# Performance work log

Hardware: AMD Instinct MI355X
Metric: run time of the kernel (lower is better)

Reference implementation:

```python
import jax, jax.numpy as jnp
import numpy as np

EPS = 1e-8

def setup_inputs() -> dict:
    key = jax.random.key(0)
    k1, k2 = jax.random.split(key)
    x = jax.random.normal(k1, (8192, 256), dtype=jnp.float32)
    y = jax.random.normal(k2, (8192, 256), dtype=jnp.float32)
    return {"x": x, "y": y}

def _compute_loss(a, b):
    # a: [N, d], b: [N, d]; sim = a @ b.T -> [N, N]
    sim = jnp.einsum('nd,md->nm', a, b)
    # log(exp(diag)/sum_j exp(sim_j)) = diag - logsumexp(row)  (same math as
    # exp -> diag/sum -> log in the original, expressed in fused stable form)
    pos = jnp.diagonal(sim)
    log_ratio = pos - jax.nn.logsumexp(sim, axis=1)
    return -jnp.sum(log_ratio)

def reference(x, y):
    x_norm = x / (jnp.linalg.norm(x, axis=1, keepdims=True) + EPS)
    y_norm = y / (jnp.linalg.norm(y, axis=1, keepdims=True) + EPS)
    loss_1 = _compute_loss(x_norm, x_norm)
    loss_2 = _compute_loss(x_norm, y_norm)
    loss_3 = _compute_loss(y_norm, y_norm)
    return loss_1 + loss_2 + loss_3
```

## Files before the change

### kernel.cpp

```cpp
#include <hip/hip_runtime.h>
#include <hip/hip_bf16.h>


#define N_ROWS 8192
#define DIM 256
#define EPSF 1e-8f
#define BM 128
#define BK 32
#define TILE (BM * BK)

typedef __attribute__((ext_vector_type(8))) short bf16x8;
typedef __attribute__((ext_vector_type(4))) float f32x4;
typedef __attribute__((ext_vector_type(4))) short short4v;

__device__ __forceinline__ short f2bf(float f) {
  unsigned u = __float_as_uint(f);
  unsigned r = (u + 0x7fffu + ((u >> 16) & 1u)) >> 16;
  return (short)r;
}

__device__ __forceinline__ float bf2f(short s) {
  return __uint_as_float(((unsigned)(unsigned short)s) << 16);
}

typedef const __attribute__((address_space(1))) void g_void;
typedef __attribute__((address_space(3))) void s_void;

__device__ __forceinline__ void gld_lds16(const void* g, void* l) {
  __builtin_amdgcn_global_load_lds((g_void*)g, (s_void*)l, 16, 0, 0);
}

__global__ void k_normalize(const float* __restrict__ x, const float* __restrict__ y,
                            short* __restrict__ xn, short* __restrict__ yn,
                            float* __restrict__ rowsum, float* __restrict__ out) {
  if (blockIdx.x < 96) rowsum[blockIdx.x * 256 + threadIdx.x] = 0.f;
  if (blockIdx.x == 96 && threadIdx.x == 0) out[0] = 0.f;

  int wave = threadIdx.x >> 6;
  int lane = threadIdx.x & 63;
  int row = blockIdx.x * 4 + wave;
  const float* src;
  short* dst;
  int r;
  if (row < N_ROWS) { src = x; dst = xn; r = row; }
  else              { src = y; dst = yn; r = row - N_ROWS; }
  const float4 v = *(const float4*)(src + r * DIM + lane * 4);
  float ss = v.x * v.x + v.y * v.y + v.z * v.z + v.w * v.w;
  #pragma unroll
  for (int m = 1; m < 64; m <<= 1) ss += __shfl_xor(ss, m, 64);
  float scale = 1.0f / (sqrtf(ss) + EPSF);
  short4v o;
  o.x = f2bf(v.x * scale);
  o.y = f2bf(v.y * scale);
  o.z = f2bf(v.z * scale);
  o.w = f2bf(v.w * scale);
  *(short4v*)(dst + r * DIM + lane * 4) = o;
}

__global__ __launch_bounds__(256, 4) void k_gemm(const short* __restrict__ xn,
                                                 const short* __restrict__ yn,
                                                 float* __restrict__ rowsum) {
  __shared__ __align__(16) short As[2 * TILE];
  __shared__ __align__(16) short Bs[2 * TILE];
  __shared__ float redbuf[256];

  int bid = blockIdx.x;
  int swz = (bid & 7) * 1032 + (bid >> 3);

  int pair, mb, nb;
  if (swz < 4160) {
    pair = (swz < 2080) ? 0 : 2;
    int t = (swz < 2080) ? swz : swz - 2080;
    int r = 0;
    while (t >= 64 - r) { t -= 64 - r; ++r; }
    mb = r; nb = r + t;
  } else {
    pair = 1;
    int t = swz - 4160;
    mb = t >> 6; nb = t & 63;
  }

  const short* Ap = (pair == 2) ? yn : xn;
  const short* Bp = (pair == 0) ? xn : yn;
  const short* Abase = Ap + mb * BM * DIM;
  const short* Bbase = Bp + nb * BM * DIM;

  int tid = threadIdx.x;
  int lane = tid & 63;
  int wid = tid >> 6;
  int wm = wid >> 1, wn = wid & 1;

  redbuf[tid] = 0.f;

  f32x4 acc[4][4];
  #pragma unroll
  for (int i = 0; i < 4; ++i)
    #pragma unroll
    for (int j = 0; j < 4; ++j) acc[i][j] = (f32x4){0.f, 0.f, 0.f, 0.f};

  auto stage = [&](int buf, int koff) {
    #pragma unroll
    for (int i = 0; i < 2; ++i) {
      int s = i * 256 + tid;
      int row = s >> 2, c = s & 3;
      int cs = c ^ (row & 3) ^ ((row >> 2) & 3);
      gld_lds16(Abase + row * DIM + koff + cs * 8, As + buf * TILE + s * 8);
      gld_lds16(Bbase + row * DIM + koff + cs * 8, Bs + buf * TILE + s * 8);
    }
  };

  int fslot = (lane >> 4) ^ (lane & 3) ^ ((lane >> 2) & 3);

  auto compute = [&](int buf) {
    bf16x8 a[4], b[4];
    #pragma unroll
    for (int mi = 0; mi < 4; ++mi) {
      int row = wm * 64 + mi * 16 + (lane & 15);
      a[mi] = *(const bf16x8*)(As + buf * TILE + row * BK + fslot * 8);
    }
    #pragma unroll
    for (int ni = 0; ni < 4; ++ni) {
      int row = wn * 64 + ni * 16 + (lane & 15);
      b[ni] = *(const bf16x8*)(Bs + buf * TILE + row * BK + fslot * 8);
    }
    #pragma unroll
    for (int mi = 0; mi < 4; ++mi)
      #pragma unroll
      for (int ni = 0; ni < 4; ++ni)
        acc[mi][ni] = __builtin_amdgcn_mfma_f32_16x16x32_bf16(a[mi], b[ni], acc[mi][ni], 0, 0, 0);
  };

  stage(0, 0);
  __syncthreads();
  #pragma unroll
  for (int ks = 0; ks < 8; ++ks) {
    if (ks < 7) stage((ks + 1) & 1, (ks + 1) * BK);
    compute(ks & 1);
    if (ks < 7) __syncthreads();
  }

  #pragma unroll
  for (int mi = 0; mi < 4; ++mi)
    #pragma unroll
    for (int ni = 0; ni < 4; ++ni)
      #pragma unroll
      for (int r = 0; r < 4; ++r)
        acc[mi][ni][r] = __expf(acc[mi][ni][r]);

  float rs[4][4];
  #pragma unroll
  for (int mi = 0; mi < 4; ++mi)
    #pragma unroll
    for (int r = 0; r < 4; ++r)
      rs[mi][r] = acc[mi][0][r] + acc[mi][1][r] + acc[mi][2][r] + acc[mi][3][r];
  #pragma unroll
  for (int m = 1; m < 16; m <<= 1)
    #pragma unroll
    for (int mi = 0; mi < 4; ++mi)
      #pragma unroll
      for (int r = 0; r < 4; ++r) rs[mi][r] += __shfl_xor(rs[mi][r], m, 64);
  if ((lane & 15) == 0) {
    int rloc = wm * 64 + (lane >> 4) * 4;
    #pragma unroll
    for (int mi = 0; mi < 4; ++mi)
      #pragma unroll
      for (int r = 0; r < 4; ++r)
        atomicAdd(&redbuf[rloc + mi * 16 + r], rs[mi][r]);
  }

  bool do_cols = (pair != 1) && (nb > mb);
  if (do_cols) {
    float cs[4];
    #pragma unroll
    for (int ni = 0; ni < 4; ++ni) {
      cs[ni] = 0.f;
      #pragma unroll
      for (int mi = 0; mi < 4; ++mi)
        #pragma unroll
        for (int r = 0; r < 4; ++r) cs[ni] += acc[mi][ni][r];
    }
    #pragma unroll
    for (int m = 16; m < 64; m <<= 1)
      #pragma unroll
      for (int ni = 0; ni < 4; ++ni) cs[ni] += __shfl_xor(cs[ni], m, 64);
    if (lane < 16) {
      #pragma unroll
      for (int ni = 0; ni < 4; ++ni)
        atomicAdd(&redbuf[128 + wn * 64 + ni * 16 + lane], cs[ni]);
    }
  }
  __syncthreads();

  if (tid < 128)
    atomicAdd(&rowsum[pair * N_ROWS + mb * BM + tid], redbuf[tid]);
  else if (do_cols)
    atomicAdd(&rowsum[pair * N_ROWS + nb * BM + (tid - 128)], redbuf[tid]);
}

__global__ void k_reduce(const short* __restrict__ xn, const short* __restrict__ yn,
                         const float* __restrict__ rowsum, float* __restrict__ out) {
  int tid = threadIdx.x, lane = tid & 63, wid = tid >> 6;
  int gw = blockIdx.x * 4 + wid;
  float acc = 0.f;
  for (int r = gw; r < 3 * N_ROWS; r += 1024) {
    int pair = r / N_ROWS;
    int n = r - pair * N_ROWS;
    const short* a = (pair == 2) ? yn : xn;
    const short* b = (pair == 0) ? xn : yn;
    short4v av = *(const short4v*)(a + n * DIM + lane * 4);
    short4v bv = *(const short4v*)(b + n * DIM + lane * 4);
    float dot = bf2f(av.x) * bf2f(bv.x) + bf2f(av.y) * bf2f(bv.y) +
                bf2f(av.z) * bf2f(bv.z) + bf2f(av.w) * bf2f(bv.w);
    #pragma unroll
    for (int m = 1; m < 64; m <<= 1) dot += __shfl_xor(dot, m, 64);
    if (lane == 0) acc += logf(rowsum[r]) - dot;
  }
  __shared__ float tmp[4];
  if (lane == 0) tmp[wid] = acc;
  __syncthreads();
  if (tid == 0) atomicAdd(out, tmp[0] + tmp[1] + tmp[2] + tmp[3]);
}

extern "C" void kernel_launch(void* const* d_in, const int* in_sizes, int n_in,
                              void* d_out, int out_size, void* d_ws, size_t ws_size,
                              hipStream_t stream) {
  const float* x = (const float*)d_in[0];
  const float* y = (const float*)d_in[1];
  short* xn = (short*)d_ws;
  short* yn = xn + N_ROWS * DIM;
  float* rowsum = (float*)(yn + N_ROWS * DIM);
  float* out = (float*)d_out;

  size_t need = (size_t)2 * N_ROWS * DIM * sizeof(short) + 3 * N_ROWS * sizeof(float);
  if (ws_size < need) return;

  k_normalize<<<4096, 256, 0, stream>>>(x, y, xn, yn, rowsum, out);
  k_gemm<<<8256, 256, 0, stream>>>(xn, yn, rowsum);
  k_reduce<<<256, 256, 0, stream>>>(xn, yn, rowsum, out);
}
```

Measured before the change: 204.9 us.

## Widen GEMM tile to 128x256 with rectangular symmetric-block enumeration

Widens the B tile from 128 to 256 columns so each block computes a 128x256 sim tile with 4x8 MFMA accumulators per wave. The triangular enumeration for the symmetric pairs is rebuilt for rectangular blocks, with masks that skip the duplicated half-tile for row and column sums. The LDS swizzle is simplified to match. The goal is more operand reuse per LDS load and about half as many blocks and atomics, at the cost of doubled accumulator registers, occupancy reduced to 2 blocks per CU, and some wasted MFMA work on diagonal tiles.

```diff
diff --git a/kernel.cpp b/kernel.cpp
--- a/kernel.cpp
+++ b/kernel.cpp
@@ -6,8 +6,10 @@
 #define DIM 256
 #define EPSF 1e-8f
 #define BM 128
+#define BN 256
 #define BK 32
-#define TILE (BM * BK)
+#define ATILE (BM * BK)
+#define BTILE (BN * BK)
 
 typedef __attribute__((ext_vector_type(8))) short bf16x8;
 typedef __attribute__((ext_vector_type(4))) float f32x4;
@@ -57,33 +59,42 @@
   *(short4v*)(dst + r * DIM + lane * 4) = o;
 }
 
-__global__ __launch_bounds__(256, 4) void k_gemm(const short* __restrict__ xn,
+__global__ __launch_bounds__(256, 2) void k_gemm(const short* __restrict__ xn,
                                                  const short* __restrict__ yn,
                                                  float* __restrict__ rowsum) {
-  __shared__ __align__(16) short As[2 * TILE];
-  __shared__ __align__(16) short Bs[2 * TILE];
-  __shared__ float redbuf[256];
+  __shared__ __align__(16) short As[2 * ATILE];
+  __shared__ __align__(16) short Bs[2 * BTILE];
+  __shared__ float redbuf[384];
 
   int bid = blockIdx.x;
-  int swz = (bid & 7) * 1032 + (bid >> 3);
+  int swz = (bid & 7) * 520 + (bid >> 3);
 
   int pair, mb, nb;
-  if (swz < 4160) {
-    pair = (swz < 2080) ? 0 : 2;
-    int t = (swz < 2080) ? swz : swz - 2080;
-    int r = 0;
-    while (t >= 64 - r) { t -= 64 - r; ++r; }
-    mb = r; nb = r + t;
+  if (swz < 2112) {
+    pair = (swz < 1056) ? 0 : 2;
+    int t = (swz < 1056) ? swz : swz - 1056;
+    int nbi = 0;
+    while (true) {
+      int cnt = 2 * nbi + 2;
+      if (t < cnt) { mb = t; break; }
+      t -= cnt; ++nbi;
+    }
+    nb = nbi;
   } else {
     pair = 1;
-    int t = swz - 4160;
-    mb = t >> 6; nb = t & 63;
-  }
+    int t = swz - 2112;
+    mb = t >> 5; nb = t & 31;
+  }
+
+  bool sym = (pair != 1);
+  bool l_row = !(sym && (mb == 2 * nb + 1));
+  bool l_col = sym && (2 * nb > mb);
+  bool r_col = sym && (2 * nb + 1 > mb);
 
   const short* Ap = (pair == 2) ? yn : xn;
   const short* Bp = (pair == 0) ? xn : yn;
   const short* Abase = Ap + mb * BM * DIM;
-  const short* Bbase = Bp + nb * BM * DIM;
+  const short* Bbase = Bp + nb * BN * DIM;
 
   int tid = threadIdx.x;
   int lane = tid & 63;
@@ -91,42 +102,49 @@
   int wm = wid >> 1, wn = wid & 1;
 
   redbuf[tid] = 0.f;
-
-  f32x4 acc[4][4];
+  if (tid < 128) redbuf[256 + tid] = 0.f;
+
+  f32x4 acc[4][8];
   #pragma unroll
   for (int i = 0; i < 4; ++i)
     #pragma unroll
-    for (int j = 0; j < 4; ++j) acc[i][j] = (f32x4){0.f, 0.f, 0.f, 0.f};
+    for (int j = 0; j < 8; ++j) acc[i][j] = (f32x4){0.f, 0.f, 0.f, 0.f};
 
   auto stage = [&](int buf, int koff) {
     #pragma unroll
     for (int i = 0; i < 2; ++i) {
       int s = i * 256 + tid;
       int row = s >> 2, c = s & 3;
-      int cs = c ^ (row & 3) ^ ((row >> 2) & 3);
-      gld_lds16(Abase + row * DIM + koff + cs * 8, As + buf * TILE + s * 8);
-      gld_lds16(Bbase + row * DIM + koff + cs * 8, Bs + buf * TILE + s * 8);
+      int cs = c ^ ((row >> 1) & 3);
+      gld_lds16(Abase + row * DIM + koff + cs * 8, As + buf * ATILE + s * 8);
+    }
+    #pragma unroll
+    for (int i = 0; i < 4; ++i) {
+      int s = i * 256 + tid;
+      int row = s >> 2, c = s & 3;
+      int cs = c ^ ((row >> 1) & 3);
+      gld_lds16(Bbase + row * DIM + koff + cs * 8, Bs + buf * BTILE + s * 8);
     }
   };
 
-  int fslot = (lane >> 4) ^ (lane & 3) ^ ((lane >> 2) & 3);
+  int fslot = (lane >> 4) ^ ((lane >> 1) & 3);
 
   auto compute = [&](int buf) {
-    bf16x8 a[4], b[4];
+    bf16x8 a[4], b[8];
     #pragma unroll
     for (int mi = 0; mi < 4; ++mi) {
       int row = wm * 64 + mi * 16 + (lane & 15);
-      a[mi] = *(const bf16x8*)(As + buf * TILE + row * BK + fslot * 8);
-    }
-    #pragma unroll
-    for (int ni = 0; ni < 4; ++ni) {
-      int row = wn * 64 + ni * 16 + (lane & 15);
-      b[ni] = *(const bf16x8*)(Bs + buf * TILE + row * BK + fslot * 8);
+      a[mi] = *(const bf16x8*)(As + buf * ATILE + row * BK + fslot * 8);
+    }
+    #pragma unroll
+    for (int ni = 0; ni < 8; ++ni) {
+      int row = wn * 128 + ni * 16 + (lane & 15);
+      b[ni] = *(const bf16x8*)(Bs + buf * BTILE + row * BK + fslot * 8);
     }
     #pragma unroll
     for (int mi = 0; mi < 4; ++mi)
       #pragma unroll
-      for (int ni = 0; ni < 4; ++ni)
+      for (int ni = 0; ni < 8; ++ni)
         acc[mi][ni] = __builtin_amdgcn_mfma_f32_16x16x32_bf16(a[mi], b[ni], acc[mi][ni], 0, 0, 0);
   };
 
@@ -142,7 +160,7 @@
   #pragma unroll
   for (int mi = 0; mi < 4; ++mi)
     #pragma unroll
-    for (int ni = 0; ni < 4; ++ni)
+    for (int ni = 0; ni < 8; ++ni)
       #pragma unroll
       for (int r = 0; r < 4; ++r)
         acc[mi][ni][r] = __expf(acc[mi][ni][r]);
@@ -151,8 +169,11 @@
   #pragma unroll
   for (int mi = 0; mi < 4; ++mi)
     #pragma unroll
-    for (int r = 0; r < 4; ++r)
-      rs[mi][r] = acc[mi][0][r] + acc[mi][1][r] + acc[mi][2][r] + acc[mi][3][r];
+    for (int r = 0; r < 4; ++r) {
+      float sl = acc[mi][0][r] + acc[mi][1][r] + acc[mi][2][r] + acc[mi][3][r];
+      float sr = acc[mi][4][r] + acc[mi][5][r] + acc[mi][6][r] + acc[mi][7][r];
+      rs[mi][r] = (l_row ? sl : 0.f) + sr;
+    }
   #pragma unroll
   for (int m = 1; m < 16; m <<= 1)
     #pragma unroll
@@ -168,33 +189,34 @@
         atomicAdd(&redbuf[rloc + mi * 16 + r], rs[mi][r]);
   }
 
-  bool do_cols = (pair != 1) && (nb > mb);
-  if (do_cols) {
-    float cs[4];
-    #pragma unroll
-    for (int ni = 0; ni < 4; ++ni) {
-      cs[ni] = 0.f;
+  if (l_col || r_col) {
+    float cs_[8];
+    #pragma unroll
+    for (int ni = 0; ni < 8; ++ni) {
+      cs_[ni] = 0.f;
       #pragma unroll
       for (int mi = 0; mi < 4; ++mi)
         #pragma unroll
-        for (int r = 0; r < 4; ++r) cs[ni] += acc[mi][ni][r];
+        for (int r = 0; r < 4; ++r) cs_[ni] += acc[mi][ni][r];
     }
     #pragma unroll
     for (int m = 16; m < 64; m <<= 1)
       #pragma unroll
-      for (int ni = 0; ni < 4; ++ni) cs[ni] += __shfl_xor(cs[ni], m, 64);
+      for (int ni = 0; ni < 8; ++ni) cs_[ni] += __shfl_xor(cs_[ni], m, 64);
     if (lane < 16) {
       #pragma unroll
-      for (int ni = 0; ni < 4; ++ni)
-        atomicAdd(&redbuf[128 + wn * 64 + ni * 16 + lane], cs[ni]);
+      for (int ni = 0; ni < 8; ++ni)
+        if (ni < 4 ? l_col : r_col)
+          atomicAdd(&redbuf[128 + wn * 128 + ni * 16 + lane], cs_[ni]);
     }
   }
   __syncthreads();
 
   if (tid < 128)
     atomicAdd(&rowsum[pair * N_ROWS + mb * BM + tid], redbuf[tid]);
-  else if (do_cols)
-    atomicAdd(&rowsum[pair * N_ROWS + nb * BM + (tid - 128)], redbuf[tid]);
+  bool cvalid = (tid < 128) ? l_col : r_col;
+  if (cvalid)
+    atomicAdd(&rowsum[pair * N_ROWS + nb * BN + tid], redbuf[128 + tid]);
 }
 
 __global__ void k_reduce(const short* __restrict__ xn, const short* __restrict__ yn,
@@ -235,6 +257,6 @@
   if (ws_size < need) return;
 
   k_normalize<<<4096, 256, 0, stream>>>(x, y, xn, yn, rowsum, out);
-  k_gemm<<<8256, 256, 0, stream>>>(xn, yn, rowsum);
+  k_gemm<<<4160, 256, 0, stream>>>(xn, yn, rowsum);
   k_reduce<<<256, 256, 0, stream>>>(xn, yn, rowsum, out);
 }
```

Result: faster. 190.0 us (-7.3%).

## Use 256x256 GEMM tiles with 4-stage async pipeline and fuse diagonal extraction

Applied to the files above, without the earlier changes.

Grows the output tile from 128x128 to 256x256 with 512-thread blocks, which halves global/LDS traffic per FLOP and cuts the block count. Replaces double buffering with a 4-deep LDS ring driven by explicit vmcnt waits and s_barrier, and raises wave priority around the MFMA block. The positive-pair diagonal sum is now taken from the accumulators in diagonal tiles, so the reduce kernel only takes logs of the row sums and no longer re-reads the normalized matrices. The cost is much higher register pressure (128 accumulator floats per lane) and larger LDS use, which lowers occupancy.

```diff
diff --git a/kernel.cpp b/kernel.cpp
--- a/kernel.cpp
+++ b/kernel.cpp
@@ -5,9 +5,10 @@
 #define N_ROWS 8192
 #define DIM 256
 #define EPSF 1e-8f
-#define BM 128
+#define BT 256
 #define BK 32
-#define TILE (BM * BK)
+#define KSTEPS 8
+#define SLOTS 2048
 
 typedef __attribute__((ext_vector_type(8))) short bf16x8;
 typedef __attribute__((ext_vector_type(4))) float f32x4;
@@ -18,14 +19,12 @@
   unsigned r = (u + 0x7fffu + ((u >> 16) & 1u)) >> 16;
   return (short)r;
 }
-
 __device__ __forceinline__ float bf2f(short s) {
   return __uint_as_float(((unsigned)(unsigned short)s) << 16);
 }
 
 typedef const __attribute__((address_space(1))) void g_void;
 typedef __attribute__((address_space(3))) void s_void;
-
 __device__ __forceinline__ void gld_lds16(const void* g, void* l) {
   __builtin_amdgcn_global_load_lds((g_void*)g, (s_void*)l, 16, 0, 0);
 }
@@ -35,13 +34,12 @@
                             float* __restrict__ rowsum, float* __restrict__ out) {
   if (blockIdx.x < 96) rowsum[blockIdx.x * 256 + threadIdx.x] = 0.f;
   if (blockIdx.x == 96 && threadIdx.x == 0) out[0] = 0.f;
+  if (blockIdx.x == 97 && threadIdx.x == 0) rowsum[3 * N_ROWS] = 0.f;
 
   int wave = threadIdx.x >> 6;
   int lane = threadIdx.x & 63;
   int row = blockIdx.x * 4 + wave;
-  const float* src;
-  short* dst;
-  int r;
+  const float* src; short* dst; int r;
   if (row < N_ROWS) { src = x; dst = xn; r = row; }
   else              { src = y; dst = yn; r = row - N_ROWS; }
   const float4 v = *(const float4*)(src + r * DIM + lane * 4);
@@ -50,119 +48,147 @@
   for (int m = 1; m < 64; m <<= 1) ss += __shfl_xor(ss, m, 64);
   float scale = 1.0f / (sqrtf(ss) + EPSF);
   short4v o;
-  o.x = f2bf(v.x * scale);
-  o.y = f2bf(v.y * scale);
-  o.z = f2bf(v.z * scale);
-  o.w = f2bf(v.w * scale);
+  o.x = f2bf(v.x * scale); o.y = f2bf(v.y * scale);
+  o.z = f2bf(v.z * scale); o.w = f2bf(v.w * scale);
   *(short4v*)(dst + r * DIM + lane * 4) = o;
 }
 
-__global__ __launch_bounds__(256, 4) void k_gemm(const short* __restrict__ xn,
+__global__ __launch_bounds__(512, 2) void k_gemm(const short* __restrict__ xn,
                                                  const short* __restrict__ yn,
                                                  float* __restrict__ rowsum) {
-  __shared__ __align__(16) short As[2 * TILE];
-  __shared__ __align__(16) short Bs[2 * TILE];
-  __shared__ float redbuf[256];
+  __shared__ __align__(16) short As[4][1024 * 8];
+  __shared__ __align__(16) short Bs[4][1024 * 8];
+  __shared__ float redbuf[512];
+  __shared__ float possum_s;
 
   int bid = blockIdx.x;
-  int swz = (bid & 7) * 1032 + (bid >> 3);
+  int swz = (bid & 7) * 260 + (bid >> 3);
 
   int pair, mb, nb;
-  if (swz < 4160) {
-    pair = (swz < 2080) ? 0 : 2;
-    int t = (swz < 2080) ? swz : swz - 2080;
+  if (swz < 1056) {
+    pair = (swz < 528) ? 0 : 2;
+    int t = (swz < 528) ? swz : swz - 528;
     int r = 0;
-    while (t >= 64 - r) { t -= 64 - r; ++r; }
+    while (t >= 32 - r) { t -= 32 - r; ++r; }
     mb = r; nb = r + t;
   } else {
     pair = 1;
-    int t = swz - 4160;
-    mb = t >> 6; nb = t & 63;
+    int t = swz - 1056;
+    mb = t >> 5; nb = t & 31;
   }
 
   const short* Ap = (pair == 2) ? yn : xn;
   const short* Bp = (pair == 0) ? xn : yn;
-  const short* Abase = Ap + mb * BM * DIM;
-  const short* Bbase = Bp + nb * BM * DIM;
+  const short* Abase = Ap + mb * BT * DIM;
+  const short* Bbase = Bp + nb * BT * DIM;
 
   int tid = threadIdx.x;
   int lane = tid & 63;
   int wid = tid >> 6;
-  int wm = wid >> 1, wn = wid & 1;
+  int wm = wid >> 2;
+  int wn = wid & 3;
 
   redbuf[tid] = 0.f;
-
-  f32x4 acc[4][4];
-  #pragma unroll
-  for (int i = 0; i < 4; ++i)
+  if (tid == 0) possum_s = 0.f;
+
+  f32x4 acc[8][4];
+  #pragma unroll
+  for (int i = 0; i < 8; ++i)
     #pragma unroll
     for (int j = 0; j < 4; ++j) acc[i][j] = (f32x4){0.f, 0.f, 0.f, 0.f};
 
-  auto stage = [&](int buf, int koff) {
+  auto stage = [&](int t) {
+    int buf = t & 3, koff = t * BK;
     #pragma unroll
     for (int i = 0; i < 2; ++i) {
-      int s = i * 256 + tid;
+      int s = i * 512 + tid;
       int row = s >> 2, c = s & 3;
-      int cs = c ^ (row & 3) ^ ((row >> 2) & 3);
-      gld_lds16(Abase + row * DIM + koff + cs * 8, As + buf * TILE + s * 8);
-      gld_lds16(Bbase + row * DIM + koff + cs * 8, Bs + buf * TILE + s * 8);
+      int cs = c ^ ((row >> 1) & 3);
+      gld_lds16(Abase + row * DIM + koff + cs * 8, &As[buf][s * 8]);
+    }
+    #pragma unroll
+    for (int i = 0; i < 2; ++i) {
+      int s = i * 512 + tid;
+      int row = s >> 2, c = s & 3;
+      int cs = c ^ ((row >> 1) & 3);
+      gld_lds16(Bbase + row * DIM + koff + cs * 8, &Bs[buf][s * 8]);
     }
   };
 
-  int fslot = (lane >> 4) ^ (lane & 3) ^ ((lane >> 2) & 3);
-
-  auto compute = [&](int buf) {
-    bf16x8 a[4], b[4];
-    #pragma unroll
-    for (int mi = 0; mi < 4; ++mi) {
-      int row = wm * 64 + mi * 16 + (lane & 15);
-      a[mi] = *(const bf16x8*)(As + buf * TILE + row * BK + fslot * 8);
+  int fslot = (lane >> 4) ^ ((lane >> 1) & 3);
+
+  auto compute = [&](int t) {
+    int buf = t & 3;
+    bf16x8 a[8], b[4];
+    #pragma unroll
+    for (int mi = 0; mi < 8; ++mi) {
+      int row = wm * 128 + mi * 16 + (lane & 15);
+      a[mi] = *(const bf16x8*)(&As[buf][row * BK + fslot * 8]);
     }
     #pragma unroll
     for (int ni = 0; ni < 4; ++ni) {
       int row = wn * 64 + ni * 16 + (lane & 15);
-      b[ni] = *(const bf16x8*)(Bs + buf * TILE + row * BK + fslot * 8);
-    }
-    #pragma unroll
-    for (int mi = 0; mi < 4; ++mi)
+      b[ni] = *(const bf16x8*)(&Bs[buf][row * BK + fslot * 8]);
+    }
+    __builtin_amdgcn_s_setprio(1);
+    #pragma unroll
+    for (int mi = 0; mi < 8; ++mi)
       #pragma unroll
       for (int ni = 0; ni < 4; ++ni)
         acc[mi][ni] = __builtin_amdgcn_mfma_f32_16x16x32_bf16(a[mi], b[ni], acc[mi][ni], 0, 0, 0);
+    __builtin_amdgcn_s_setprio(0);
   };
 
-  stage(0, 0);
-  __syncthreads();
-  #pragma unroll
-  for (int ks = 0; ks < 8; ++ks) {
-    if (ks < 7) stage((ks + 1) & 1, (ks + 1) * BK);
-    compute(ks & 1);
-    if (ks < 7) __syncthreads();
-  }
-
-  #pragma unroll
-  for (int mi = 0; mi < 4; ++mi)
+  stage(0); stage(1); stage(2);
+
+#define ITER(T, VM)                                                      \
+  asm volatile("s_waitcnt vmcnt(" #VM ")\n\ts_barrier" ::: "memory");    \
+  if ((T) + 3 < KSTEPS) stage((T) + 3);                                  \
+  compute(T);
+  ITER(0, 8) ITER(1, 8) ITER(2, 8) ITER(3, 8) ITER(4, 8) ITER(5, 8)
+  ITER(6, 4) ITER(7, 0)
+#undef ITER
+
+  bool diag = (mb == nb);
+  if (diag) {
+    float ps = 0.f;
+    #pragma unroll
+    for (int mi = 0; mi < 8; ++mi)
+      #pragma unroll
+      for (int ni = 0; ni < 4; ++ni)
+        #pragma unroll
+        for (int r = 0; r < 4; ++r) {
+          int rr = wm * 128 + mi * 16 + (lane >> 4) * 4 + r;
+          int cc = wn * 64 + ni * 16 + (lane & 15);
+          if (rr == cc) ps += acc[mi][ni][r];
+        }
+    if (ps != 0.f) atomicAdd(&possum_s, ps);
+  }
+
+  #pragma unroll
+  for (int mi = 0; mi < 8; ++mi)
     #pragma unroll
     for (int ni = 0; ni < 4; ++ni)
       #pragma unroll
       for (int r = 0; r < 4; ++r)
         acc[mi][ni][r] = __expf(acc[mi][ni][r]);
 
-  float rs[4][4];
-  #pragma unroll
-  for (int mi = 0; mi < 4; ++mi)
+  float rs[8][4];
+  #pragma unroll
+  for (int mi = 0; mi < 8; ++mi)
     #pragma unroll
     for (int r = 0; r < 4; ++r)
       rs[mi][r] = acc[mi][0][r] + acc[mi][1][r] + acc[mi][2][r] + acc[mi][3][r];
   #pragma unroll
   for (int m = 1; m < 16; m <<= 1)
     #pragma unroll
-    for (int mi = 0; mi < 4; ++mi)
+    for (int mi = 0; mi < 8; ++mi)
       #pragma unroll
       for (int r = 0; r < 4; ++r) rs[mi][r] += __shfl_xor(rs[mi][r], m, 64);
   if ((lane & 15) == 0) {
-    int rloc = wm * 64 + (lane >> 4) * 4;
-    #pragma unroll
-    for (int mi = 0; mi < 4; ++mi)
+    int rloc = wm * 128 + (lane >> 4) * 4;
+    #pragma unroll
+    for (int mi = 0; mi < 8; ++mi)
       #pragma unroll
       for (int r = 0; r < 4; ++r)
         atomicAdd(&redbuf[rloc + mi * 16 + r], rs[mi][r]);
@@ -175,7 +201,7 @@
     for (int ni = 0; ni < 4; ++ni) {
       cs[ni] = 0.f;
       #pragma unroll
-      for (int mi = 0; mi < 4; ++mi)
+      for (int mi = 0; mi < 8; ++mi)
         #pragma unroll
         for (int r = 0; r < 4; ++r) cs[ni] += acc[mi][ni][r];
     }
@@ -186,39 +212,32 @@
     if (lane < 16) {
       #pragma unroll
       for (int ni = 0; ni < 4; ++ni)
-        atomicAdd(&redbuf[128 + wn * 64 + ni * 16 + lane], cs[ni]);
+        atomicAdd(&redbuf[256 + wn * 64 + ni * 16 + lane], cs[ni]);
     }
   }
   __syncthreads();
 
-  if (tid < 128)
-    atomicAdd(&rowsum[pair * N_ROWS + mb * BM + tid], redbuf[tid]);
+  if (tid < 256)
+    atomicAdd(&rowsum[pair * N_ROWS + mb * BT + tid], redbuf[tid]);
   else if (do_cols)
-    atomicAdd(&rowsum[pair * N_ROWS + nb * BM + (tid - 128)], redbuf[tid]);
-}
-
-__global__ void k_reduce(const short* __restrict__ xn, const short* __restrict__ yn,
-                         const float* __restrict__ rowsum, float* __restrict__ out) {
+    atomicAdd(&rowsum[pair * N_ROWS + nb * BT + (tid - 256)], redbuf[tid]);
+  if (tid == 0 && diag && possum_s != 0.f)
+    atomicAdd(&rowsum[3 * N_ROWS], possum_s);
+}
+
+__global__ void k_reduce(const float* __restrict__ rowsum, float* __restrict__ out) {
   int tid = threadIdx.x, lane = tid & 63, wid = tid >> 6;
-  int gw = blockIdx.x * 4 + wid;
-  float acc = 0.f;
-  for (int r = gw; r < 3 * N_ROWS; r += 1024) {
-    int pair = r / N_ROWS;
-    int n = r - pair * N_ROWS;
-    const short* a = (pair == 2) ? yn : xn;
-    const short* b = (pair == 0) ? xn : yn;
-    short4v av = *(const short4v*)(a + n * DIM + lane * 4);
-    short4v bv = *(const short4v*)(b + n * DIM + lane * 4);
-    float dot = bf2f(av.x) * bf2f(bv.x) + bf2f(av.y) * bf2f(bv.y) +
-                bf2f(av.z) * bf2f(bv.z) + bf2f(av.w) * bf2f(bv.w);
-    #pragma unroll
-    for (int m = 1; m < 64; m <<= 1) dot += __shfl_xor(dot, m, 64);
-    if (lane == 0) acc += logf(rowsum[r]) - dot;
-  }
+  float v = logf(rowsum[blockIdx.x * 256 + tid]);
+  #pragma unroll
+  for (int m = 1; m < 64; m <<= 1) v += __shfl_xor(v, m, 64);
   __shared__ float tmp[4];
-  if (lane == 0) tmp[wid] = acc;
+  if (lane == 0) tmp[wid] = v;
   __syncthreads();
-  if (tid == 0) atomicAdd(out, tmp[0] + tmp[1] + tmp[2] + tmp[3]);
+  if (tid == 0) {
+    float s = tmp[0] + tmp[1] + tmp[2] + tmp[3];
+    if (blockIdx.x == 0) s -= rowsum[3 * N_ROWS];
+    atomicAdd(out, s);
+  }
 }
 
 extern "C" void kernel_launch(void* const* d_in, const int* in_sizes, int n_in,
@@ -231,10 +250,10 @@
   float* rowsum = (float*)(yn + N_ROWS * DIM);
   float* out = (float*)d_out;
 
-  size_t need = (size_t)2 * N_ROWS * DIM * sizeof(short) + 3 * N_ROWS * sizeof(float);
+  size_t need = (size_t)2 * N_ROWS * DIM * sizeof(short) + (3 * N_ROWS + 1) * sizeof(float);
   if (ws_size < need) return;
 
   k_normalize<<<4096, 256, 0, stream>>>(x, y, xn, yn, rowsum, out);
-  k_gemm<<<8256, 256, 0, stream>>>(xn, yn, rowsum);
-  k_reduce<<<256, 256, 0, stream>>>(xn, yn, rowsum, out);
-}
+  k_gemm<<<2080, 512, 0, stream>>>(xn, yn, rowsum);
+  k_reduce<<<96, 256, 0, stream>>>(rowsum, out);
+}
```

After: 189.3 us. 1.08x faster.
